# Optimization experiments

Hardware: AMD Instinct MI355X
Metric: run time of the kernel (lower is better)

The kernel has to match this reference:

```python
import jax, jax.numpy as jnp
import numpy as np

NUM_CODE = 1024
CODE_DIM = 256


def setup_inputs() -> dict:
    key = jax.random.key(0)
    k1, k2 = jax.random.split(key)
    z_e = jax.random.normal(k1, (32, CODE_DIM, 32, 32), dtype=jnp.float32)
    span = 1.0 / NUM_CODE
    codebook = jax.random.uniform(k2, (NUM_CODE, CODE_DIM), dtype=jnp.float32,
                                  minval=-span, maxval=span)
    return {"z_e": z_e, "codebook": codebook}


def reference(z_e, codebook):
    # NCHW -> NHWC
    z = jnp.transpose(z_e, (0, 2, 3, 1))  # [B,H,W,D]
    B, H, W, D = z.shape
    zf = z.reshape(-1, D)  # [N,D]
    cb = jax.lax.stop_gradient(codebook)
    # squared L2 distances via sum-sq + matmul
    d = (jnp.sum(zf * zf, axis=1, keepdims=True)
         + jnp.sum(cb * cb, axis=1)
         - 2.0 * jnp.einsum('nd,kd->nk', zf, cb))  # [N,K]
    indices = jnp.argmin(d, axis=1)  # [N]
    z_q = cb[indices].reshape(B, H, W, D)
    # straight-through estimator
    z_q = z + jax.lax.stop_gradient(z_q - z)
    indices = indices.reshape(B, H, W)
    z_q = jnp.transpose(z_q, (0, 3, 1, 2))  # back to NCHW
    return z_q, indices
```

## Files before the change

### kernel.cpp

```cpp
#include <hip/hip_runtime.h>

#define D_   256
#define HW_  1024
#define N_   32768
#define K_   1024

#define QMARGS 0.12288f

typedef _Float16 half8 __attribute__((ext_vector_type(8)));
typedef __attribute__((ext_vector_type(4))) float f32x4;

#define GLDS(g, l) __builtin_amdgcn_global_load_lds( \
    (const __attribute__((address_space(1))) unsigned int*)(g), \
    (__attribute__((address_space(3))) unsigned int*)(l), 16, 0, 0)


__device__ __forceinline__ float np_sumsq_256(const float* a, int stride) {
    float blk[2];
    #pragma unroll
    for (int h = 0; h < 2; ++h) {
        const float* p = a + (size_t)h * 128 * stride;
        float r[8];
        #pragma unroll
        for (int j = 0; j < 8; ++j) {
            float v = p[(size_t)j * stride];
            r[j] = __fmul_rn(v, v);
        }
        for (int i = 1; i < 16; ++i) {
            #pragma unroll
            for (int j = 0; j < 8; ++j) {
                float v = p[(size_t)(i * 8 + j) * stride];
                r[j] = __fadd_rn(r[j], __fmul_rn(v, v));
            }
        }
        blk[h] = __fadd_rn(__fadd_rn(__fadd_rn(r[0], r[1]), __fadd_rn(r[2], r[3])),
                           __fadd_rn(__fadd_rn(r[4], r[5]), __fadd_rn(r[6], r[7])));
    }
    return __fadd_rn(blk[0], blk[1]);
}

__global__ __launch_bounds__(256) void prep_kernel(const float* __restrict__ z,
                                                   const float* __restrict__ cb,
                                                   float* __restrict__ A32,
                                                   float* __restrict__ B32,
                                                   float* __restrict__ hbF,
                                                   half8* __restrict__ cbAf,
                                                   half8* __restrict__ zBf) {
    const int blk = blockIdx.x;
    const int tid = threadIdx.x;
    if (blk < 4) {
        int k = blk * 256 + tid;
        float v = np_sumsq_256(cb + (size_t)k * D_, 1);
        B32[k] = v;
        hbF[k] = 512.0f * v;
    } else if (blk < 132) {
        int n  = (blk - 4) * 256 + tid;
        int b  = n >> 10;
        int hw = n & 1023;
        A32[n] = np_sumsq_256(z + (size_t)b * (D_ * HW_) + hw, HW_);
    } else if (blk < 260) {
        int c  = (blk - 132) * 256 + tid;
        int kf = c >> 9;
        int ds = (c >> 6) & 7;
        int q  = (c >> 4) & 3;
        int r  = c & 15;
        int k  = kf * 16 + r;
        int d0 = ds * 32 + q * 8;
        const float* src = cb + (size_t)k * D_ + d0;
        half8 v;
        #pragma unroll
        for (int j = 0; j < 8; ++j) v[j] = (_Float16)(src[j] * -1024.0f);
        cbAf[c] = v;
    } else {
        int c    = (blk - 260) * 256 + tid;
        int pxg  = c >> 9;
        int ds   = (c >> 6) & 7;
        int lane = c & 63;
        int q    = lane >> 4;
        int r    = lane & 15;
        int px   = pxg * 16 + r;
        int bb   = px >> 10;
        int hw   = px & 1023;
        int d0   = ds * 32 + q * 8;
        const float* src = z + (size_t)bb * (D_ * HW_) + hw;
        half8 v;
        #pragma unroll
        for (int j = 0; j < 8; ++j) v[j] = (_Float16)src[(size_t)(d0 + j) * HW_];
        zBf[c] = v;
    }
}

#define CSWAP(va, ka, vb, kb) { \
    bool sw = (vb < va) || (vb == va && kb < ka); \
    float tv = va; int tk = ka; \
    va = sw ? vb : va; ka = sw ? kb : ka; \
    vb = sw ? tv : vb; kb = sw ? tk : kb; }

#define TOP4_INS(S, KK, V0,K0,V1,K1,V2,K2,V3,K3) \
    if (S < V3) { \
        if (S < V1) { \
            V3 = V2; K3 = K2; V2 = V1; K2 = K1; \
            if (S < V0) { V1 = V0; K1 = K0; V0 = S; K0 = KK; } \
            else        { V1 = S;  K1 = KK; } \
        } else { \
            if (S < V2) { V3 = V2; K3 = K2; V2 = S; K2 = KK; } \
            else        { V3 = S;  K3 = KK; } \
        } \
    }

#define QMERGE(V0,K0,V1,K1,V2,K2,V3,K3) \
    _Pragma("unroll") \
    for (int off = 16; off <= 32; off <<= 1) { \
        float b0_ = __shfl_xor(V0, off, 64), b1_ = __shfl_xor(V1, off, 64); \
        float b2_ = __shfl_xor(V2, off, 64), b3_ = __shfl_xor(V3, off, 64); \
        int   c0_ = __shfl_xor(K0, off, 64), c1_ = __shfl_xor(K1, off, 64); \
        int   c2_ = __shfl_xor(K2, off, 64), c3_ = __shfl_xor(K3, off, 64); \
        CSWAP(V0, K0, b3_, c3_); CSWAP(V1, K1, b2_, c2_); \
        CSWAP(V2, K2, b1_, c1_); CSWAP(V3, K3, b0_, c0_); \
        CSWAP(V0, K0, V2, K2); CSWAP(V1, K1, V3, K3); \
        CSWAP(V0, K0, V1, K1); CSWAP(V2, K2, V3, K3); \
    }

#define MERGE2(V0,K0,V1,K1,V2,K2,V3,K3, W0,P0,W1,P1,W2,P2,W3,P3) { \
    CSWAP(V0, K0, W3, P3); CSWAP(V1, K1, W2, P2); \
    CSWAP(V2, K2, W1, P1); CSWAP(V3, K3, W0, P0); \
    CSWAP(V0, K0, V2, K2); CSWAP(V1, K1, V3, K3); \
    CSWAP(V0, K0, V1, K1); CSWAP(V2, K2, V3, K3); }

__global__ __launch_bounds__(256, 6) void vq_screen16(
        const half8* __restrict__ zBf,
        const half8* __restrict__ cbAf,
        const float* __restrict__ hbF,
        float* __restrict__ st4)
{
    __shared__ half8 abuf[2][512];

    const int tid  = threadIdx.x;
    const int lane = tid & 63;
    const int wave = tid >> 6;
    const int q    = lane >> 4;
    const int r    = lane & 15;

    const int x    = blockIdx.x & 7;
    const int g    = blockIdx.x >> 3;
    const int tile = x * 64 + (g >> 3);
    const int k8   = g & 7;

    const int f0 = tile * 4 + wave;
    half8 b0[8];
    #pragma unroll
    for (int ds = 0; ds < 8; ++ds)
        b0[ds] = zBf[(size_t)(f0 * 8 + ds) * 64 + lane];

    const char* gbase = (const char*)cbAf + (size_t)k8 * 65536
                      + wave * 2048 + lane * 16;
    const int   ldsOff = wave * 128;

    {
        char* d = (char*)&abuf[0][ldsOff];
        GLDS(gbase, d);
        GLDS(gbase + 1024, d + 1024);
    }
    __syncthreads();

    float v0 = 3.4e38f, v1 = 3.4e38f, v2 = 3.4e38f, v3 = 3.4e38f;
    int   k0 = 0x7fffffff, k1 = 0x7fffffff, k2 = 0x7fffffff, k3 = 0x7fffffff;

    for (int chl = 0; chl < 8; ++chl) {
        const int cur = chl & 1;
        if (chl < 7) {
            const char* s = gbase + (size_t)(chl + 1) * 8192;
            char* d = (char*)&abuf[cur ^ 1][ldsOff];
            GLDS(s, d);
            GLDS(s + 1024, d + 1024);
        }

        const int kbase = k8 * 128 + chl * 16;
        const float4 h = *reinterpret_cast<const float4*>(&hbF[kbase + q * 4]);
        f32x4 acc = {h.x, h.y, h.z, h.w};

        #pragma unroll
        for (int ds = 0; ds < 8; ++ds) {
            half8 A0 = abuf[cur][ds * 64 + lane];
            acc = __builtin_amdgcn_mfma_f32_16x16x32_f16(A0, b0[ds], acc, 0,0,0);
        }

        float mg = fminf(fminf(acc[0], acc[1]), fminf(acc[2], acc[3]));
        if (mg < v3) {
            #pragma unroll
            for (int i = 0; i < 4; ++i) {
                int kk  = kbase + q * 4 + i;
                float s = acc[i];
                TOP4_INS(s, kk, v0,k0, v1,k1, v2,k2, v3,k3);
            }
        }
        __syncthreads();
    }

    QMERGE(v0,k0, v1,k1, v2,k2, v3,k3);

    if (q == 0) {
        int n = tile * 64 + wave * 16 + r;
        float* p = st4 + ((size_t)k8 * N_ + n) * 8;
        *reinterpret_cast<float4*>(p)     = make_float4(v0, v1, v2, v3);
        *reinterpret_cast<float4*>(p + 4) = make_float4(
            __int_as_float(k0), __int_as_float(k1),
            __int_as_float(k2), __int_as_float(k3));
    }
}

__global__ __launch_bounds__(256) void finish_kernel(
        const float* __restrict__ st4,
        const float* __restrict__ A32,
        const float* __restrict__ B32,
        const float* __restrict__ cb,
        const float* __restrict__ z,
        float* __restrict__ oidx,
        float* __restrict__ zq)
{
    __shared__ int fcount;
    __shared__ int flist[64];
    __shared__ int fck[64][4];
    __shared__ int fidx[64];

    const int tid  = threadIdx.x;
    const int lane = tid & 63;
    const int wave = tid >> 6;
    const int p0   = blockIdx.x * 64;

    if (tid == 0) fcount = 0;
    __syncthreads();

    if (tid < 64) {
        const int n = p0 + tid;
        float V0, V1, V2, V3; int K0, K1, K2, K3;
        {
            const float* p = st4 + (size_t)n * 8;
            float4 v  = *reinterpret_cast<const float4*>(p);
            float4 kf = *reinterpret_cast<const float4*>(p + 4);
            V0 = v.x; V1 = v.y; V2 = v.z; V3 = v.w;
            K0 = __float_as_int(kf.x); K1 = __float_as_int(kf.y);
            K2 = __float_as_int(kf.z); K3 = __float_as_int(kf.w);
        }
        #pragma unroll
        for (int k8 = 1; k8 < 8; ++k8) {
            const float* p = st4 + ((size_t)k8 * N_ + n) * 8;
            float4 v  = *reinterpret_cast<const float4*>(p);
            float4 kf = *reinterpret_cast<const float4*>(p + 4);
            float W0 = v.x, W1 = v.y, W2 = v.z, W3 = v.w;
            int   P0 = __float_as_int(kf.x), P1 = __float_as_int(kf.y);
            int   P2 = __float_as_int(kf.z), P3 = __float_as_int(kf.w);
            MERGE2(V0,K0, V1,K1, V2,K2, V3,K3, W0,P0, W1,P1, W2,P2, W3,P3);
        }
        fidx[tid] = K0;
        oidx[n] = (float)K0;
        if (V1 - V0 < QMARGS) {
            int slot = atomicAdd(&fcount, 1);
            flist[slot] = tid;
            fck[slot][0] = K0; fck[slot][1] = K1;
            fck[slot][2] = K2; fck[slot][3] = K3;
        }
    }
    __syncthreads();

    const int fc = fcount;
    for (int i = wave; i < fc; i += 4) {
        const int pl = flist[i];
        const int nn = p0 + pl;
        const int bb = nn >> 10, hw = nn & 1023;
        const float* zb = z + (size_t)bb * (D_ * HW_) + hw;
        float zf[4];
        #pragma unroll
        for (int j = 0; j < 4; ++j) zf[j] = zb[(size_t)(lane * 4 + j) * HW_];

        const float An = A32[nn];
        float bd = 3.4e38f;
        int   bk = 0x7fffffff;
        #pragma unroll
        for (int c = 0; c < 4; ++c) {
            int k = fck[i][c];
            float4 c4 = *reinterpret_cast<const float4*>(cb + (size_t)k * D_ + lane * 4);
            double acc = 0.0;
            acc = fma((double)c4.x, (double)zf[0], acc);
            acc = fma((double)c4.y, (double)zf[1], acc);
            acc = fma((double)c4.z, (double)zf[2], acc);
            acc = fma((double)c4.w, (double)zf[3], acc);
            #pragma unroll
            for (int off = 1; off <= 32; off <<= 1) acc += __shfl_xor(acc, off, 64);
            float C32 = (float)acc;
            float d32 = __fsub_rn(__fadd_rn(An, B32[k]), __fadd_rn(C32, C32));
            if (d32 < bd || (d32 == bd && k < bk)) { bd = d32; bk = k; }
        }
        if (lane == 0) { oidx[nn] = (float)bk; fidx[pl] = bk; }
    }
    __syncthreads();

    if (p0 >= 16384 && p0 < 24576) return;
    const int s_nl = tid & 63;
    const int s_dw = tid >> 6;
    const int b    = p0 >> 10;
    const int hw0  = p0 & 1023;
    const int idxn = fidx[s_nl];
    const float4* crow = reinterpret_cast<const float4*>(cb + (size_t)idxn * D_);
    float* zqb = zq + (size_t)b * (D_ * HW_) + hw0;
    #pragma unroll
    for (int rr = 0; rr < 16; ++rr) {
        int d4 = s_dw * 16 + rr;
        float4 c4 = crow[d4];
        int d = d4 * 4;
        zqb[(size_t)(d + 0) * HW_ + s_nl] = c4.x;
        zqb[(size_t)(d + 1) * HW_ + s_nl] = c4.y;
        zqb[(size_t)(d + 2) * HW_ + s_nl] = c4.z;
        zqb[(size_t)(d + 3) * HW_ + s_nl] = c4.w;
    }
}

__global__ __launch_bounds__(256) void gather2_kernel(const float* __restrict__ cb,
                                                      const float* __restrict__ oidx,
                                                      float* __restrict__ zq,
                                                      int base) {
    const int tid  = threadIdx.x;
    const int s_nl = tid & 63;
    const int s_dw = tid >> 6;
    const int p0   = base + blockIdx.x * 64;
    const int b    = p0 >> 10;
    const int hw0  = p0 & 1023;

    int idxn = (int)oidx[p0 + s_nl];
    const float4* crow = reinterpret_cast<const float4*>(cb + (size_t)idxn * D_);
    float* zqb = zq + (size_t)b * (D_ * HW_) + hw0;
    #pragma unroll
    for (int r = 0; r < 16; ++r) {
        int d4 = s_dw * 16 + r;
        float4 c4 = crow[d4];
        int d = d4 * 4;
        zqb[(size_t)(d + 0) * HW_ + s_nl] = c4.x;
        zqb[(size_t)(d + 1) * HW_ + s_nl] = c4.y;
        zqb[(size_t)(d + 2) * HW_ + s_nl] = c4.z;
        zqb[(size_t)(d + 3) * HW_ + s_nl] = c4.w;
    }
}

extern "C" void kernel_launch(void* const* d_in, const int* in_sizes, int n_in,
                              void* d_out, int out_size, void* d_ws, size_t ws_size,
                              hipStream_t stream) {
    const float* z  = (const float*)d_in[0];
    const float* cb = (const float*)d_in[1];

    float* zq   = (float*)d_out;
    float* oidx = zq + (size_t)N_ * D_;

    char* ws = (char*)d_ws;
    float* B32  = (float*)(ws + 0);
    float* hbF  = (float*)(ws + 4096);
    float* A32  = (float*)(ws + 8192);
    half8* cbAf = (half8*)(ws + 139264);

    char*  zqb = (char*)zq;
    half8* zBf = (half8*)zqb;
    float* st4 = (float*)(zqb + 16777216);

    prep_kernel<<<4356, 256, 0, stream>>>(z, cb, A32, B32, hbF, cbAf, zBf);
    vq_screen16<<<4096, 256, 0, stream>>>(zBf, cbAf, hbF, st4);
    finish_kernel<<<N_ / 64, 256, 0, stream>>>(st4, A32, B32, cb, z, oidx, zq);
    gather2_kernel<<<128, 256, 0, stream>>>(cb, oidx, zq, 16384);
}
```

Baseline: 92.04 us.

## Transpose z through LDS in prep and move candidate buffer to workspace

The prep kernel now stages a 16-pixel by 256-channel tile of z in shared memory once, then computes the per-pixel sum of squares and the fp16 packed layout from that tile, so z is no longer read twice with strided loads. When the workspace is large enough, the top-4 candidate buffer lives in the workspace instead of aliasing the output. finish_kernel can then write all outputs directly and the extra gather kernel launch is skipped. This depends on ws_size at runtime, and if the workspace is too small the old shadowed path is kept.

New measurement: 76.73 us. 1.2x faster.

```diff
diff --git a/kernel.cpp b/kernel.cpp
--- a/kernel.cpp
+++ b/kernel.cpp
@@ -54,12 +54,7 @@
         B32[k] = v;
         hbF[k] = 512.0f * v;
     } else if (blk < 132) {
-        int n  = (blk - 4) * 256 + tid;
-        int b  = n >> 10;
-        int hw = n & 1023;
-        A32[n] = np_sumsq_256(z + (size_t)b * (D_ * HW_) + hw, HW_);
-    } else if (blk < 260) {
-        int c  = (blk - 132) * 256 + tid;
+        int c  = (blk - 4) * 256 + tid;
         int kf = c >> 9;
         int ds = (c >> 6) & 7;
         int q  = (c >> 4) & 3;
@@ -72,21 +67,39 @@
         for (int j = 0; j < 8; ++j) v[j] = (_Float16)(src[j] * -1024.0f);
         cbAf[c] = v;
     } else {
-        int c    = (blk - 260) * 256 + tid;
-        int pxg  = c >> 9;
-        int ds   = (c >> 6) & 7;
-        int lane = c & 63;
-        int q    = lane >> 4;
-        int r    = lane & 15;
-        int px   = pxg * 16 + r;
-        int bb   = px >> 10;
-        int hw   = px & 1023;
-        int d0   = ds * 32 + q * 8;
-        const float* src = z + (size_t)bb * (D_ * HW_) + hw;
-        half8 v;
-        #pragma unroll
-        for (int j = 0; j < 8; ++j) v[j] = (_Float16)src[(size_t)(d0 + j) * HW_];
-        zBf[c] = v;
+        __shared__ float zt[16][257];
+        const int pxg = blk - 132;
+        const int px0 = pxg * 16;
+        const int bb  = px0 >> 10;
+        const int hw0 = px0 & 1023;
+        const float* zb = z + (size_t)bb * (D_ * HW_) + hw0;
+
+        {
+            const int r  = tid & 15;
+            const int dg = tid >> 4;
+            #pragma unroll
+            for (int j = 0; j < 16; ++j) {
+                int d = j * 16 + dg;
+                zt[r][d] = zb[(size_t)d * HW_ + r];
+            }
+        }
+        __syncthreads();
+
+        if (tid < 16) A32[px0 + tid] = np_sumsq_256(&zt[tid][0], 1);
+
+        #pragma unroll
+        for (int h = 0; h < 2; ++h) {
+            int cl   = h * 256 + tid;
+            int ds   = cl >> 6;
+            int lane = cl & 63;
+            int q    = lane >> 4;
+            int rr   = lane & 15;
+            int d0   = ds * 32 + q * 8;
+            half8 v;
+            #pragma unroll
+            for (int j = 0; j < 8; ++j) v[j] = (_Float16)zt[rr][d0 + j];
+            zBf[(size_t)pxg * 512 + cl] = v;
+        }
     }
 }
 
@@ -216,7 +229,8 @@
         const float* __restrict__ cb,
         const float* __restrict__ z,
         float* __restrict__ oidx,
-        float* __restrict__ zq)
+        float* __restrict__ zq,
+        int shadow)
 {
     __shared__ int fcount;
     __shared__ int flist[64];
@@ -295,7 +309,7 @@
     }
     __syncthreads();
 
-    if (p0 >= 16384 && p0 < 24576) return;
+    if (shadow && p0 >= 16384 && p0 < 24576) return;
     const int s_nl = tid & 63;
     const int s_dw = tid >> 6;
     const int b    = p0 >> 10;
@@ -358,10 +372,16 @@
 
     char*  zqb = (char*)zq;
     half8* zBf = (half8*)zqb;
-    float* st4 = (float*)(zqb + 16777216);
-
-    prep_kernel<<<4356, 256, 0, stream>>>(z, cb, A32, B32, hbF, cbAf, zBf);
+
+    const size_t ST4_BYTES = (size_t)8 * N_ * 32;
+    bool ws_big = ws_size >= (size_t)663552 + ST4_BYTES;
+    float* st4  = ws_big ? (float*)(ws + 663552)
+                         : (float*)(zqb + 16777216);
+    int shadow  = ws_big ? 0 : 1;
+
+    prep_kernel<<<2180, 256, 0, stream>>>(z, cb, A32, B32, hbF, cbAf, zBf);
     vq_screen16<<<4096, 256, 0, stream>>>(zBf, cbAf, hbF, st4);
-    finish_kernel<<<N_ / 64, 256, 0, stream>>>(st4, A32, B32, cb, z, oidx, zq);
-    gather2_kernel<<<128, 256, 0, stream>>>(cb, oidx, zq, 16384);
-}
+    finish_kernel<<<N_ / 64, 256, 0, stream>>>(st4, A32, B32, cb, z, oidx, zq, shadow);
+    if (shadow)
+        gather2_kernel<<<128, 256, 0, stream>>>(cb, oidx, zq, 16384);
+}
```
